# Kernel optimization log

Measured on AMD Instinct MI355X. Metric: run time of the kernel, lower is better.

## Reference

```python
import jax, jax.numpy as jnp
import numpy as np
import math

D_MODEL = 1024
NUM_HEADS = 16
D_K = D_MODEL // NUM_HEADS
THETA = 10000.0
NEG_INF = 1.0e6  # module uses -1e6, not -inf


def _rope_tables(seq_len):
    pair_idx = jnp.arange(0, D_K, 2, dtype=jnp.float32)
    inv_freq = 1.0 / (THETA ** (pair_idx / D_K))
    pos = jnp.arange(seq_len, dtype=jnp.float32)
    angles = jnp.outer(pos, inv_freq)  # (S, D_K//2)
    return jnp.cos(angles), jnp.sin(angles)


def _apply_rope(x, cos, sin):
    # x: (B, H, S, D_K); cos/sin: (S, D_K//2)
    xe = x[..., 0::2]
    xo = x[..., 1::2]
    oe = xe * cos - xo * sin
    oo = xe * sin + xo * cos
    return jnp.stack([oe, oo], axis=-1).reshape(x.shape)


def setup_inputs() -> dict:
    key = jax.random.key(0)
    k0, k1, k2, k3, k4 = jax.random.split(key, 5)
    B, S = 2, 2048
    x = jax.random.normal(k0, (B, S, D_MODEL), dtype=jnp.float32)
    scale = 0.02
    wq = jax.random.normal(k1, (D_MODEL, D_MODEL), dtype=jnp.float32) * scale
    wk = jax.random.normal(k2, (D_MODEL, D_MODEL), dtype=jnp.float32) * scale
    wv = jax.random.normal(k3, (D_MODEL, D_MODEL), dtype=jnp.float32) * scale
    wo = jax.random.normal(k4, (D_MODEL, D_MODEL), dtype=jnp.float32) * scale
    return {"x": x, "wq": wq, "wk": wk, "wv": wv, "wo": wo}


def reference(x, wq, wk, wv, wo):
    B, S, _ = x.shape
    q = x @ wq.T
    k = x @ wk.T
    v = x @ wv.T
    # (B, S, H, d_k) -> (B, H, S, d_k)
    q = q.reshape(B, S, NUM_HEADS, D_K).transpose(0, 2, 1, 3)
    k = k.reshape(B, S, NUM_HEADS, D_K).transpose(0, 2, 1, 3)
    v = v.reshape(B, S, NUM_HEADS, D_K).transpose(0, 2, 1, 3)
    cos, sin = _rope_tables(S)
    q = _apply_rope(q, cos, sin)
    k = _apply_rope(k, cos, sin)
    scores = jnp.einsum("bhqd,bhkd->bhqk", q, k) / math.sqrt(D_K)
    causal = jnp.tril(jnp.ones((S, S), dtype=bool))
    scores = jnp.where(causal, scores, -NEG_INF)
    attn = jax.nn.softmax(scores, axis=-1)
    out = jnp.einsum("bhqk,bhkd->bhqd", attn, v)
    out = out.transpose(0, 2, 1, 3).reshape(B, S, D_MODEL)
    return out @ wo.T
```

## Files before the change

kernel.cpp:

```cpp
#include <hip/hip_runtime.h>

typedef __attribute__((ext_vector_type(8))) __bf16 bf16x8;
typedef __attribute__((ext_vector_type(8))) _Float16 f16x8;
typedef __attribute__((ext_vector_type(4))) float f32x4;
typedef __attribute__((ext_vector_type(8))) unsigned short u16x8;
typedef __attribute__((ext_vector_type(4))) unsigned int u32x4;

#define MFMA_BF16(a, b, c) __builtin_amdgcn_mfma_f32_16x16x32_bf16((a), (b), (c), 0, 0, 0)
#define MFMA_F16(a, b, c)  __builtin_amdgcn_mfma_f32_16x16x32_f16((a), (b), (c), 0, 0, 0)
#define LOG2E 1.44269504088896340736f
#define QSCALE 0.18033688011112042f

__device__ __forceinline__ float b2f(unsigned short u) {
    union { unsigned int i; float f; } v; v.i = ((unsigned int)u) << 16; return v.f;
}
__device__ __forceinline__ unsigned short f2bf(float f) {
    union { float f; unsigned int i; } v; v.f = f;
    unsigned int u = v.i;
    return (unsigned short)((u + 0x7fffu + ((u >> 16) & 1u)) >> 16);
}

__device__ __forceinline__ void gl_lds16(const void* g, void* l) {
    __builtin_amdgcn_global_load_lds(
        (const __attribute__((address_space(1))) void*)g,
        (__attribute__((address_space(3))) void*)l,
        16, 0, 0);
}

__global__ __launch_bounds__(256) void cvt_all(const float* __restrict__ x,
                                               const float* __restrict__ wq,
                                               const float* __restrict__ wk,
                                               const float* __restrict__ wv,
                                               const float* __restrict__ wo,
                                               unsigned short* __restrict__ xb,
                                               unsigned short* __restrict__ wqb,
                                               unsigned short* __restrict__ wkb,
                                               unsigned short* __restrict__ wvb,
                                               unsigned short* __restrict__ wob) {
    int id = blockIdx.x * 256 + threadIdx.x;
    const float* src; unsigned short* dst; size_t off; float scl = 1.0f;
    if (id < 524288)      { src = x;  dst = xb;  off = (size_t)id * 8; }
    else if (id < 655360) { src = wq; dst = wqb; off = (size_t)(id - 524288) * 8; scl = QSCALE; }
    else if (id < 786432) { src = wk; dst = wkb; off = (size_t)(id - 655360) * 8; }
    else if (id < 917504) { src = wv; dst = wvb; off = (size_t)(id - 786432) * 8; }
    else                  { src = wo; dst = wob; off = (size_t)(id - 917504) * 8; }
    float4 a = *(const float4*)(src + off);
    float4 b = *(const float4*)(src + off + 4);
    u16x8 o;
    o[0] = f2bf(a.x * scl); o[1] = f2bf(a.y * scl); o[2] = f2bf(a.z * scl); o[3] = f2bf(a.w * scl);
    o[4] = f2bf(b.x * scl); o[5] = f2bf(b.y * scl); o[6] = f2bf(b.z * scl); o[7] = f2bf(b.w * scl);
    *(u16x8*)(dst + off) = o;
}

template <int MODE>
__device__ __forceinline__ void gemm128_bt(const unsigned short* __restrict__ A,
                                           const unsigned short* __restrict__ B,
                                           void* __restrict__ Cv,
                                           int m0, int n0, int ldc,
                                           unsigned short* As, unsigned short* Bs) {
    const int tid = threadIdx.x;
    const int w = tid >> 6, lane = tid & 63;
    const int quad = lane >> 4, l15 = lane & 15;
    const int wm = w & 1, wn = w >> 1;

    f32x4 acc[4][4];
#pragma unroll
    for (int mt = 0; mt < 4; ++mt)
#pragma unroll
        for (int nt = 0; nt < 4; ++nt) acc[mt][nt] = f32x4{0.f, 0.f, 0.f, 0.f};

    for (int k0 = 0; k0 < 1024; k0 += 32) {
        __syncthreads();
#pragma unroll
        for (int i = 0; i < 2; ++i) {
            int L = (w * 2 + i) * 64 + lane;
            int r = L >> 2;
            int c = (L & 3) ^ ((r >> 1) & 3);
            gl_lds16(A + (size_t)(m0 + r) * 1024 + k0 + c * 8, As + L * 8);
            gl_lds16(B + (size_t)(n0 + r) * 1024 + k0 + c * 8, Bs + L * 8);
        }
        __syncthreads();

        bf16x8 af[4], bfr[4];
#pragma unroll
        for (int mt = 0; mt < 4; ++mt) {
            int row = wm * 64 + mt * 16 + l15;
            af[mt] = *(const bf16x8*)(As + row * 32 + (quad ^ ((row >> 1) & 3)) * 8);
        }
#pragma unroll
        for (int nt = 0; nt < 4; ++nt) {
            int row = wn * 64 + nt * 16 + l15;
            bfr[nt] = *(const bf16x8*)(Bs + row * 32 + (quad ^ ((row >> 1) & 3)) * 8);
        }
#pragma unroll
        for (int mt = 0; mt < 4; ++mt)
#pragma unroll
            for (int nt = 0; nt < 4; ++nt)
                acc[mt][nt] = MFMA_BF16(af[mt], bfr[nt], acc[mt][nt]);
    }

    float invf[4], sgn = 0.f;
    if constexpr (MODE == 3) {
        sgn = (l15 & 1) ? 1.0f : -1.0f;
#pragma unroll
        for (int nt = 0; nt < 4; ++nt)
            invf[nt] = exp2f(-0.41524101186092029f * (float)((nt * 16 + l15) >> 1));
    }

#pragma unroll
    for (int mt = 0; mt < 4; ++mt) {
        int grow = m0 + wm * 64 + mt * 16 + quad * 4;
#pragma unroll
        for (int nt = 0; nt < 4; ++nt) {
            int gcol = n0 + wn * 64 + nt * 16 + l15;
#pragma unroll
            for (int r = 0; r < 4; ++r) {
                float val = acc[mt][nt][r];
                size_t idx = (size_t)(grow + r) * ldc + gcol;
                if constexpr (MODE == 0) {
                    ((unsigned short*)Cv)[idx] = f2bf(val);
                } else if constexpr (MODE == 1) {
                    ((float*)Cv)[idx] = val;
                } else if constexpr (MODE == 2) {
                    _Float16 hv = (_Float16)val;
                    ((unsigned short*)Cv)[idx] = __builtin_bit_cast(unsigned short, hv);
                } else {
                    float p = __shfl_xor(val, 1);
                    float pos = (float)((grow + r) & 2047);
                    float ang = pos * invf[nt];
                    float out = val * __cosf(ang) + sgn * p * __sinf(ang);
                    ((unsigned short*)Cv)[idx] = f2bf(out);
                }
            }
        }
    }
}

__global__ __launch_bounds__(256) void gemm_qkv(const unsigned short* __restrict__ X,
                                                const unsigned short* __restrict__ Wq,
                                                const unsigned short* __restrict__ Wk,
                                                const unsigned short* __restrict__ Wv,
                                                unsigned short* __restrict__ Qo,
                                                unsigned short* __restrict__ Ko,
                                                unsigned short* __restrict__ Vt) {
    __shared__ unsigned short As[128 * 32];
    __shared__ unsigned short Bs[128 * 32];
    int y = blockIdx.y;
    if (y < 16) {
        int sel = y >> 3;
        int m0 = blockIdx.x * 128;
        int n0 = (y & 7) * 128;
        const unsigned short* B = sel ? Wk : Wq;
        unsigned short* C = sel ? Ko : Qo;
        gemm128_bt<3>(X, B, C, m0, n0, 1024, As, Bs);
    } else {
        int m0 = (y & 7) * 128;
        int n0 = blockIdx.x * 128;
        gemm128_bt<2>(Wv, X, Vt, m0, n0, 4096, As, Bs);
    }
}

__global__ __launch_bounds__(256) void gemm_out(const unsigned short* __restrict__ A,
                                                const unsigned short* __restrict__ Wo,
                                                float* __restrict__ C) {
    __shared__ unsigned short As[128 * 32];
    __shared__ unsigned short Bs[128 * 32];
    gemm128_bt<1>(A, Wo, C, blockIdx.x * 128, blockIdx.y * 128, 1024, As, Bs);
}

#define FBODY(MASKED)                                                                   \
    {                                                                                   \
        bf16x8 kf[4][2];                                                                \
        _Pragma("unroll")                                                               \
        for (int nt = 0; nt < 4; ++nt) {                                                \
            int row = nt * 16 + l15;                                                    \
            const unsigned short* kp = Ksb + row * 64;                                  \
            int swk = row & 7;                                                          \
            kf[nt][0] = *(const bf16x8*)(kp + (quad ^ swk) * 8);                        \
            kf[nt][1] = *(const bf16x8*)(kp + ((quad ^ 4) ^ swk) * 8);                  \
        }                                                                               \
        f16x8 pa[2][2];                                                                 \
        _Pragma("unroll")                                                               \
        for (int mt = 0; mt < 2; ++mt) {                                                \
            f32x4 sc[4];                                                                \
            _Pragma("unroll")                                                           \
            for (int nt = 0; nt < 4; ++nt) {                                            \
                f32x4 z = f32x4{0.f, 0.f, 0.f, 0.f};                                    \
                z = MFMA_BF16(kf[nt][0], qf[mt][0], z);                                 \
                sc[nt] = MFMA_BF16(kf[nt][1], qf[mt][1], z);                            \
            }                                                                           \
            int qpos = qposw + mt * 16 + l15;                                           \
            unsigned pk[8];                                                             \
            _Pragma("unroll")                                                           \
            for (int nt = 0; nt < 4; ++nt) {                                            \
                float e[4];                                                             \
                _Pragma("unroll")                                                       \
                for (int r = 0; r < 4; ++r) {                                           \
                    float ev = exp2f(sc[nt][r]);                                        \
                    if (MASKED) {                                                       \
                        int kpos = kb * 64 + nt * 16 + quad * 4 + r;                    \
                        ev = (kpos > qpos) ? 0.f : ev;                                  \
                    }                                                                   \
                    e[r] = ev;                                                          \
                }                                                                       \
                pk[nt * 2 + 0] = __builtin_bit_cast(unsigned,                           \
                                     __builtin_amdgcn_cvt_pkrtz(e[0], e[1]));           \
                pk[nt * 2 + 1] = __builtin_bit_cast(unsigned,                           \
                                     __builtin_amdgcn_cvt_pkrtz(e[2], e[3]));           \
            }                                                                           \
            u32x4 rs0 = u32x4{pk[0], pk[1], pk[2], pk[3]};                              \
            u32x4 rs1 = u32x4{pk[4], pk[5], pk[6], pk[7]};                              \
            lacc[mt] = MFMA_F16(__builtin_bit_cast(f16x8, rs0), ones, lacc[mt]);        \
            lacc[mt] = MFMA_F16(__builtin_bit_cast(f16x8, rs1), ones, lacc[mt]);        \
            int b0 = quad & 1;                                                          \
            unsigned y0 = (unsigned)__builtin_amdgcn_ds_swizzle(                        \
                              (int)(b0 ? pk[0] : pk[2]), 0x401F);                       \
            unsigned y1 = (unsigned)__builtin_amdgcn_ds_swizzle(                        \
                              (int)(b0 ? pk[1] : pk[3]), 0x401F);                       \
            unsigned y2 = (unsigned)__builtin_amdgcn_ds_swizzle(                        \
                              (int)(b0 ? pk[4] : pk[6]), 0x401F);                       \
            unsigned y3 = (unsigned)__builtin_amdgcn_ds_swizzle(                        \
                              (int)(b0 ? pk[5] : pk[7]), 0x401F);                       \
            u32x4 t0 = b0 ? u32x4{y0, y1, pk[2], pk[3]}                                 \
                          : u32x4{pk[0], pk[1], y0, y1};                                \
            u32x4 t1 = b0 ? u32x4{y2, y3, pk[6], pk[7]}                                 \
                          : u32x4{pk[4], pk[5], y2, y3};                                \
            pa[mt][0] = __builtin_bit_cast(f16x8, t0);                                  \
            pa[mt][1] = __builtin_bit_cast(f16x8, t1);                                  \
        }                                                                               \
        _Pragma("unroll")                                                               \
        for (int nt = 0; nt < 4; ++nt) {                                                \
            int rowd = nt * 16 + l15;                                                   \
            const unsigned short* vp = Vsb + rowd * 64;                                 \
            int sl0 = pi4 ^ (rowd & 7);                                                 \
            f16x8 v0 = *(const f16x8*)(vp + sl0 * 8);                                   \
            f16x8 v1 = *(const f16x8*)(vp + (sl0 ^ 4) * 8);                             \
            accO[0][nt] = MFMA_F16(pa[0][0], v0, accO[0][nt]);                          \
            accO[1][nt] = MFMA_F16(pa[1][0], v0, accO[1][nt]);                          \
            accO[0][nt] = MFMA_F16(pa[0][1], v1, accO[0][nt]);                          \
            accO[1][nt] = MFMA_F16(pa[1][1], v1, accO[1][nt]);                          \
        }                                                                               \
    }

__global__ __launch_bounds__(256) void flash_attn(const unsigned short* __restrict__ Q,
                                                  const unsigned short* __restrict__ Kb,
                                                  const unsigned short* __restrict__ Vt,
                                                  unsigned short* __restrict__ O) {
    int id = blockIdx.x;
    int xcd = id & 7;
    int s  = id >> 3;
    int rr = s & 3;
    int t  = s >> 2;
    int qt = (t < 8) ? t : 23 - t;
    int bh = xcd + 8 * rr;
    int b = bh >> 4, h = bh & 15;
    int tid = threadIdx.x, w = tid >> 6, lane = tid & 63;
    int quad = lane >> 4, l15 = lane & 15;
    int pi4 = ((quad & 1) << 1) | (quad >> 1);

    __shared__ unsigned short Ks[2 * 4096];
    __shared__ unsigned short Vs[2 * 4096];

    int L0 = w * 128 + lane;
    int L1 = L0 + 64;
    int r0 = L0 >> 3, c0 = (L0 & 7) ^ (r0 & 7);
    int r1 = L1 >> 3, c1 = (L1 & 7) ^ (r1 & 7);
    const unsigned short* Kg0 = Kb + (size_t)(b * 2048 + r0) * 1024 + h * 64 + c0 * 8;
    const unsigned short* Kg1 = Kb + (size_t)(b * 2048 + r1) * 1024 + h * 64 + c1 * 8;
    const unsigned short* Vg0 = Vt + (size_t)(h * 64 + r0) * 4096 + b * 2048 + c0 * 8;
    const unsigned short* Vg1 = Vt + (size_t)(h * 64 + r1) * 4096 + b * 2048 + c1 * 8;

    f16x8 ones;
#pragma unroll
    for (int tt = 0; tt < 8; ++tt) ones[tt] = (_Float16)1.0f;

#define STAGE(kb_, buf_)                                                    \
    {                                                                       \
        size_t ko = (size_t)(kb_) * 64 * 1024;                              \
        size_t vo = (size_t)(kb_) * 64;                                     \
        unsigned short* kd = Ks + (buf_) * 4096;                            \
        unsigned short* vd = Vs + (buf_) * 4096;                            \
        gl_lds16(Kg0 + ko, kd + L0 * 8);                                    \
        gl_lds16(Kg1 + ko, kd + L1 * 8);                                    \
        gl_lds16(Vg0 + vo, vd + L0 * 8);                                    \
        gl_lds16(Vg1 + vo, vd + L1 * 8);                                    \
    }

    int qrow0 = b * 2048 + qt * 128 + w * 32;
    int qposw = qt * 128 + w * 32;
    int nkb = 2 * qt + 2;

    STAGE(0, 0)

    bf16x8 qf[2][2];
#pragma unroll
    for (int mt = 0; mt < 2; ++mt) {
        const unsigned short* qp =
            Q + (size_t)(qrow0 + mt * 16 + l15) * 1024 + h * 64 + quad * 8;
        qf[mt][0] = *(const bf16x8*)qp;
        qf[mt][1] = *(const bf16x8*)(qp + 32);
    }

    f32x4 accO[2][4];
    f32x4 lacc[2];
#pragma unroll
    for (int mt = 0; mt < 2; ++mt) {
        lacc[mt] = f32x4{0.f, 0.f, 0.f, 0.f};
#pragma unroll
        for (int nt = 0; nt < 4; ++nt) accO[mt][nt] = f32x4{0.f, 0.f, 0.f, 0.f};
    }

    __asm__ volatile("s_waitcnt vmcnt(0)" ::: "memory");
    __builtin_amdgcn_s_barrier();
    __builtin_amdgcn_sched_barrier(0);

    int cur = 0;
    for (int kb = 0; kb < nkb; ++kb) {
        if (kb + 1 < nkb) STAGE(kb + 1, cur ^ 1)
        const unsigned short* Ksb = Ks + cur * 4096;
        const unsigned short* Vsb = Vs + cur * 4096;
        if (kb < nkb - 2) {
            FBODY(0)
        } else {
            FBODY(1)
        }
        __asm__ volatile("s_waitcnt vmcnt(0)" ::: "memory");
        __builtin_amdgcn_s_barrier();
        __builtin_amdgcn_sched_barrier(0);
        cur ^= 1;
    }

#pragma unroll
    for (int mt = 0; mt < 2; ++mt) {
        float inv[4];
#pragma unroll
        for (int r = 0; r < 4; ++r) inv[r] = 1.0f / lacc[mt][r];
#pragma unroll
        for (int nt = 0; nt < 4; ++nt)
#pragma unroll
            for (int r = 0; r < 4; ++r)
                O[(size_t)(qrow0 + mt * 16 + quad * 4 + r) * 1024 +
                  h * 64 + nt * 16 + l15] = f2bf(accO[mt][nt][r] * inv[r]);
    }
#undef STAGE
}

extern "C" void kernel_launch(void* const* d_in, const int* in_sizes, int n_in,
                              void* d_out, int out_size, void* d_ws, size_t ws_size,
                              hipStream_t stream) {
    (void)in_sizes; (void)n_in; (void)out_size; (void)ws_size;
    const float* x  = (const float*)d_in[0];
    const float* wq = (const float*)d_in[1];
    const float* wk = (const float*)d_in[2];
    const float* wv = (const float*)d_in[3];
    const float* wo = (const float*)d_in[4];
    float* out = (float*)d_out;

    const size_t T = (size_t)4096 * 1024;
    const size_t W = (size_t)1024 * 1024;
    unsigned short* Q   = (unsigned short*)d_ws;
    unsigned short* K   = Q + T;
    unsigned short* Vt  = K + T;
    unsigned short* xb  = Vt + T;
    unsigned short* AO  = xb;
    unsigned short* wqb = xb + T;
    unsigned short* wkb = wqb + W;
    unsigned short* wvb = wkb + W;
    unsigned short* wob = wvb + W;

    cvt_all  <<<dim3(4096),   256, 0, stream>>>(x, wq, wk, wv, wo, xb, wqb, wkb, wvb, wob);
    gemm_qkv <<<dim3(32, 24), 256, 0, stream>>>(xb, wqb, wkb, wvb, Q, K, Vt);
    flash_attn<<<dim3(512),   256, 0, stream>>>(Q, K, Vt, AO);
    gemm_out <<<dim3(32, 8),  256, 0, stream>>>(AO, wob, out);
}
```

Measured before the change: 190.5 us.

## Split attention KV loop across two wave groups with LDS reduction

```diff
diff --git a/kernel.cpp b/kernel.cpp
--- a/kernel.cpp
+++ b/kernel.cpp
@@ -168,7 +168,7 @@
     gemm128_bt<1>(A, Wo, C, blockIdx.x * 128, blockIdx.y * 128, 1024, As, Bs);
 }
 
-#define FBODY(MASKED)                                                                   \
+#define FBODY(KBASE, MASKED)                                                            \
     {                                                                                   \
         bf16x8 kf[4][2];                                                                \
         _Pragma("unroll")                                                               \
@@ -195,13 +195,13 @@
             for (int nt = 0; nt < 4; ++nt) {                                            \
                 float e[4];                                                             \
                 _Pragma("unroll")                                                       \
-                for (int r = 0; r < 4; ++r) {                                           \
-                    float ev = exp2f(sc[nt][r]);                                        \
+                for (int r_ = 0; r_ < 4; ++r_) {                                        \
+                    float ev = exp2f(sc[nt][r_]);                                       \
                     if (MASKED) {                                                       \
-                        int kpos = kb * 64 + nt * 16 + quad * 4 + r;                    \
+                        int kpos = (KBASE) + nt * 16 + quad * 4 + r_;                   \
                         ev = (kpos > qpos) ? 0.f : ev;                                  \
                     }                                                                   \
-                    e[r] = ev;                                                          \
+                    e[r_] = ev;                                                         \
                 }                                                                       \
                 pk[nt * 2 + 0] = __builtin_bit_cast(unsigned,                           \
                                      __builtin_amdgcn_cvt_pkrtz(e[0], e[1]));           \
@@ -242,10 +242,10 @@
         }                                                                               \
     }
 
-__global__ __launch_bounds__(256) void flash_attn(const unsigned short* __restrict__ Q,
-                                                  const unsigned short* __restrict__ Kb,
-                                                  const unsigned short* __restrict__ Vt,
-                                                  unsigned short* __restrict__ O) {
+__global__ __launch_bounds__(512, 4) void flash_attn(const unsigned short* __restrict__ Q,
+                                                     const unsigned short* __restrict__ Kb,
+                                                     const unsigned short* __restrict__ Vt,
+                                                     unsigned short* __restrict__ O) {
     int id = blockIdx.x;
     int xcd = id & 7;
     int s  = id >> 3;
@@ -254,43 +254,25 @@
     int qt = (t < 8) ? t : 23 - t;
     int bh = xcd + 8 * rr;
     int b = bh >> 4, h = bh & 15;
-    int tid = threadIdx.x, w = tid >> 6, lane = tid & 63;
+    int tid = threadIdx.x;
+    int wv8 = tid >> 6;
+    int g = wv8 >> 2;
+    int w = wv8 & 3;
+    int lane = tid & 63;
     int quad = lane >> 4, l15 = lane & 15;
     int pi4 = ((quad & 1) << 1) | (quad >> 1);
 
-    __shared__ unsigned short Ks[2 * 4096];
-    __shared__ unsigned short Vs[2 * 4096];
-
-    int L0 = w * 128 + lane;
-    int L1 = L0 + 64;
-    int r0 = L0 >> 3, c0 = (L0 & 7) ^ (r0 & 7);
-    int r1 = L1 >> 3, c1 = (L1 & 7) ^ (r1 & 7);
-    const unsigned short* Kg0 = Kb + (size_t)(b * 2048 + r0) * 1024 + h * 64 + c0 * 8;
-    const unsigned short* Kg1 = Kb + (size_t)(b * 2048 + r1) * 1024 + h * 64 + c1 * 8;
-    const unsigned short* Vg0 = Vt + (size_t)(h * 64 + r0) * 4096 + b * 2048 + c0 * 8;
-    const unsigned short* Vg1 = Vt + (size_t)(h * 64 + r1) * 4096 + b * 2048 + c1 * 8;
-
-    f16x8 ones;
-#pragma unroll
-    for (int tt = 0; tt < 8; ++tt) ones[tt] = (_Float16)1.0f;
-
-#define STAGE(kb_, buf_)                                                    \
-    {                                                                       \
-        size_t ko = (size_t)(kb_) * 64 * 1024;                              \
-        size_t vo = (size_t)(kb_) * 64;                                     \
-        unsigned short* kd = Ks + (buf_) * 4096;                            \
-        unsigned short* vd = Vs + (buf_) * 4096;                            \
-        gl_lds16(Kg0 + ko, kd + L0 * 8);                                    \
-        gl_lds16(Kg1 + ko, kd + L1 * 8);                                    \
-        gl_lds16(Vg0 + vo, vd + L0 * 8);                                    \
-        gl_lds16(Vg1 + vo, vd + L1 * 8);                                    \
-    }
+    __shared__ __align__(16) float Red[10240];
+    unsigned short* Ks = (unsigned short*)Red;
+    unsigned short* Vs = Ks + 8192;
+
+    int r = tid >> 3, c = (tid & 7) ^ (r & 7);
+    const unsigned short* KgT = Kb + (size_t)(b * 2048 + r) * 1024 + h * 64 + c * 8;
+    const unsigned short* VgT = Vt + (size_t)(h * 64 + r) * 4096 + b * 2048 + c * 8;
 
     int qrow0 = b * 2048 + qt * 128 + w * 32;
     int qposw = qt * 128 + w * 32;
-    int nkb = 2 * qt + 2;
-
-    STAGE(0, 0)
+    int nit = qt + 1;
 
     bf16x8 qf[2][2];
 #pragma unroll
@@ -301,6 +283,10 @@
         qf[mt][1] = *(const bf16x8*)(qp + 32);
     }
 
+    f16x8 ones;
+#pragma unroll
+    for (int tt = 0; tt < 8; ++tt) ones[tt] = (_Float16)1.0f;
+
     f32x4 accO[2][4];
     f32x4 lacc[2];
 #pragma unroll
@@ -310,39 +296,64 @@
         for (int nt = 0; nt < 4; ++nt) accO[mt][nt] = f32x4{0.f, 0.f, 0.f, 0.f};
     }
 
-    __asm__ volatile("s_waitcnt vmcnt(0)" ::: "memory");
-    __builtin_amdgcn_s_barrier();
-    __builtin_amdgcn_sched_barrier(0);
-
-    int cur = 0;
-    for (int kb = 0; kb < nkb; ++kb) {
-        if (kb + 1 < nkb) STAGE(kb + 1, cur ^ 1)
-        const unsigned short* Ksb = Ks + cur * 4096;
-        const unsigned short* Vsb = Vs + cur * 4096;
-        if (kb < nkb - 2) {
-            FBODY(0)
+    for (int it = 0; it < nit; ++it) {
+        __syncthreads();
+        {
+            size_t ko = (size_t)(it * 128) * 1024;
+            int vo = it * 128;
+            gl_lds16(KgT + ko, Ks + tid * 8);
+            gl_lds16(KgT + ko + 64 * 1024, Ks + 4096 + tid * 8);
+            gl_lds16(VgT + vo, Vs + tid * 8);
+            gl_lds16(VgT + vo + 64, Vs + 4096 + tid * 8);
+        }
+        __syncthreads();
+        const unsigned short* Ksb = Ks + g * 4096;
+        const unsigned short* Vsb = Vs + g * 4096;
+        int kbase = it * 128 + g * 64;
+        if (it < nit - 1) {
+            FBODY(kbase, 0)
         } else {
-            FBODY(1)
-        }
-        __asm__ volatile("s_waitcnt vmcnt(0)" ::: "memory");
-        __builtin_amdgcn_s_barrier();
-        __builtin_amdgcn_sched_barrier(0);
-        cur ^= 1;
-    }
-
-#pragma unroll
-    for (int mt = 0; mt < 2; ++mt) {
-        float inv[4];
-#pragma unroll
-        for (int r = 0; r < 4; ++r) inv[r] = 1.0f / lacc[mt][r];
-#pragma unroll
-        for (int nt = 0; nt < 4; ++nt)
-#pragma unroll
-            for (int r = 0; r < 4; ++r)
-                O[(size_t)(qrow0 + mt * 16 + quad * 4 + r) * 1024 +
-                  h * 64 + nt * 16 + l15] = f2bf(accO[mt][nt][r] * inv[r]);
-    }
-#undef STAGE
+            FBODY(kbase, 1)
+        }
+    }
+
+    __syncthreads();
+    if (g == 1) {
+        float* dst = Red + (w * 64 + lane) * 32;
+#pragma unroll
+        for (int mt = 0; mt < 2; ++mt)
+#pragma unroll
+            for (int nt = 0; nt < 4; ++nt)
+                *(f32x4*)(dst + mt * 16 + nt * 4) = accO[mt][nt];
+        float* dl = Red + 8192 + (w * 64 + lane) * 8;
+        *(f32x4*)(dl)     = lacc[0];
+        *(f32x4*)(dl + 4) = lacc[1];
+    }
+    __syncthreads();
+    if (g == 0) {
+        const float* src = Red + (w * 64 + lane) * 32;
+#pragma unroll
+        for (int mt = 0; mt < 2; ++mt)
+#pragma unroll
+            for (int nt = 0; nt < 4; ++nt)
+                accO[mt][nt] += *(const f32x4*)(src + mt * 16 + nt * 4);
+        const float* dl = Red + 8192 + (w * 64 + lane) * 8;
+        lacc[0] += *(const f32x4*)(dl);
+        lacc[1] += *(const f32x4*)(dl + 4);
+
+#pragma unroll
+        for (int mt = 0; mt < 2; ++mt) {
+            float inv[4];
+#pragma unroll
+            for (int r_ = 0; r_ < 4; ++r_) inv[r_] = 1.0f / lacc[mt][r_];
+#pragma unroll
+            for (int nt = 0; nt < 4; ++nt)
+#pragma unroll
+                for (int r_ = 0; r_ < 4; ++r_)
+                    O[(size_t)(qrow0 + mt * 16 + quad * 4 + r_) * 1024 +
+                      h * 64 + nt * 16 + l15] = f2bf(accO[mt][nt][r_] * inv[r_]);
+        }
+    }
 }
 
 extern "C" void kernel_launch(void* const* d_in, const int* in_sizes, int n_in,
@@ -370,6 +381,6 @@
 
     cvt_all  <<<dim3(4096),   256, 0, stream>>>(x, wq, wk, wv, wo, xb, wqb, wkb, wvb, wob);
     gemm_qkv <<<dim3(32, 24), 256, 0, stream>>>(xb, wqb, wkb, wvb, Q, K, Vt);
-    flash_attn<<<dim3(512),   256, 0, stream>>>(Q, K, Vt, AO);
+    flash_attn<<<dim3(512),   512, 0, stream>>>(Q, K, Vt, AO);
     gemm_out <<<dim3(32, 8),  256, 0, stream>>>(AO, wob, out);
 }
```

Result: faster. 181.4 us (-4.8%).
